# Kernel optimization log

Measured on AMD Instinct MI355X. Metric: run time of the kernel, lower is better.

## Reference

```python
import jax, jax.numpy as jnp
import numpy as np

N_NODES = 50000
N_EDGES = 800000
D_FEAT = 96


def setup_inputs() -> dict:
    key = jax.random.key(0)
    kx, ks, kd = jax.random.split(key, 3)
    x = jax.random.normal(kx, (N_NODES, D_FEAT), dtype=jnp.float32)
    src = jax.random.randint(ks, (N_EDGES,), 0, N_NODES, dtype=jnp.int64)
    dst = jax.random.randint(kd, (N_EDGES,), 0, N_NODES, dtype=jnp.int64)
    return {"x": x, "src": src, "dst": dst}


def reference(x, src, dst):
    n = x.shape[0]
    ones = jnp.ones(src.shape[0], dtype=x.dtype)
    # out-degree: edges leaving each node (src side)
    out_deg = jnp.clip(jax.ops.segment_sum(ones, src, num_segments=n), 1.0, None)
    # in-degree: edges arriving at each node (dst side)
    in_deg = jnp.clip(jax.ops.segment_sum(ones, dst, num_segments=n), 1.0, None)
    # pre-scale by out-degree^{-1/2}
    xs = x * (out_deg ** -0.5)[:, None]
    # copy_u + sum aggregation: sum messages from src into dst
    agg = jax.ops.segment_sum(xs[src], dst, num_segments=n)
    # post-scale by in-degree^{-1/2}
    return agg * (in_deg ** -0.5)[:, None]
```

## Files before the change

### kernel.cpp

```cpp
#include <hip/hip_runtime.h>


#define D_FEAT 96
#define CAP 64
#define PART_SHIFT 8
#define PNODES 256
#define NP_MAX 256
#define EPB 3328
#define EREG 13
#define OVF_CAP 8192

__device__ __forceinline__ unsigned short f2bf_rne(float f) {
    unsigned u = __float_as_uint(f);
    unsigned r = (u >> 16) & 1u;
    u += 0x7fffu + r;
    return (unsigned short)(u >> 16);
}


__global__ __launch_bounds__(256) void partition_kernel(
        const int* __restrict__ src, const int* __restrict__ dst,
        int n_edges, int np, int stride,
        int* __restrict__ pcur_d, int* __restrict__ pcur_s,
        unsigned* __restrict__ pbuf_d, unsigned short* __restrict__ pbuf_s,
        int* __restrict__ ctr,
        int* __restrict__ povf_d, int* __restrict__ sovf_d) {
    __shared__ int hcd[NP_MAX], hcs[NP_MAX];
    __shared__ int bd[NP_MAX], bs_[NP_MAX];
    __shared__ int od[NP_MAX], os_[NP_MAX];
    const int base = blockIdx.x * EPB;

    for (int i = threadIdx.x; i < NP_MAX; i += 256) {
        hcd[i] = 0; hcs[i] = 0; od[i] = 0; os_[i] = 0;
    }
    __syncthreads();

    unsigned v[EREG];
    #pragma unroll
    for (int k = 0; k < EREG; ++k) {
        int i = base + (int)threadIdx.x + (k << 8);
        if (i < n_edges) {
            int s = src[i], d = dst[i];
            unsigned pv = (unsigned)d | ((unsigned)s << 16);
            v[k] = pv;
            atomicAdd(&hcd[d >> PART_SHIFT], 1);
            atomicAdd(&hcs[s >> PART_SHIFT], 1);
        }
    }
    __syncthreads();

    for (int p = threadIdx.x; p < np; p += 256) {
        int cd = hcd[p];
        bd[p] = cd ? atomicAdd(&pcur_d[p], cd) : 0;
        int cs = hcs[p];
        bs_[p] = cs ? atomicAdd(&pcur_s[p], cs) : 0;
    }
    __syncthreads();

    #pragma unroll
    for (int k = 0; k < EREG; ++k) {
        int i = base + (int)threadIdx.x + (k << 8);
        if (i < n_edges) {
            unsigned pv = v[k];
            int d = (int)(pv & 0xffffu);
            int s = (int)(pv >> 16);
            int pd = d >> PART_SHIFT;
            int j = bd[pd] + atomicAdd(&od[pd], 1);
            if (j < stride) pbuf_d[(size_t)pd * stride + j] = pv;
            else { int k2 = atomicAdd(&ctr[1], 1); if (k2 < OVF_CAP) povf_d[k2] = (int)pv; }
            int ps = s >> PART_SHIFT;
            int j2 = bs_[ps] + atomicAdd(&os_[ps], 1);
            if (j2 < stride) pbuf_s[(size_t)ps * stride + j2] = (unsigned short)s;
            else { int k3 = atomicAdd(&ctr[2], 1); if (k3 < OVF_CAP) sovf_d[k3] = s; }
        }
    }
}


__global__ __launch_bounds__(256) void bincnt_kernel(
        const unsigned* __restrict__ pbuf_d, const int* __restrict__ pcur_d,
        const unsigned short* __restrict__ pbuf_s, const int* __restrict__ pcur_s,
        int stride, int n_nodes,
        const float* __restrict__ x, unsigned* __restrict__ xs,
        int* __restrict__ cursor, int* __restrict__ out_cnt,
        unsigned short* __restrict__ slots,
        int* __restrict__ ctr,
        const int* __restrict__ povf_d, const int* __restrict__ sovf_d,
        int* __restrict__ ovf_d) {
    __shared__ unsigned short lslots[PNODES * CAP];
    __shared__ int lcnt[PNODES];
    __shared__ int lout[PNODES];
    const int b = blockIdx.x;
    const int nbase = b << PART_SHIFT;
    const int nloc = min(PNODES, n_nodes - nbase);

    for (int i = threadIdx.x; i < PNODES; i += 256) { lcnt[i] = 0; lout[i] = 0; }
    __syncthreads();

    int n = pcur_d[b]; if (n > stride) n = stride;
    for (int i = threadIdx.x; i < n; i += 256) {
        unsigned pv = pbuf_d[(size_t)b * stride + i];
        int dl = (int)(pv & 0xffu);
        int s  = (int)(pv >> 16);
        int pos = atomicAdd(&lcnt[dl], 1);
        if (pos < CAP) lslots[dl * CAP + pos] = (unsigned short)s;
        else { int k = atomicAdd(&ctr[0], 1); if (k < OVF_CAP) ovf_d[k] = (int)pv; }
    }
    int n2 = pcur_s[b]; if (n2 > stride) n2 = stride;
    for (int i = threadIdx.x; i < n2; i += 256) {
        int s = (int)pbuf_s[(size_t)b * stride + i];
        atomicAdd(&lout[s & (PNODES - 1)], 1);
    }
    int npv = ctr[1];
    if (npv > 0) {
        if (npv > OVF_CAP) npv = OVF_CAP;
        for (int i = threadIdx.x; i < npv; i += 256) {
            unsigned pv = (unsigned)povf_d[i];
            int d = (int)(pv & 0xffffu);
            if ((d >> PART_SHIFT) == b) {
                int dl = d & (PNODES - 1);
                int pos = atomicAdd(&lcnt[dl], 1);
                if (pos < CAP) lslots[dl * CAP + pos] = (unsigned short)(pv >> 16);
                else { int k = atomicAdd(&ctr[0], 1); if (k < OVF_CAP) ovf_d[k] = (int)pv; }
            }
        }
    }
    int nsv = ctr[2];
    if (nsv > 0) {
        if (nsv > OVF_CAP) nsv = OVF_CAP;
        for (int i = threadIdx.x; i < nsv; i += 256) {
            int s = sovf_d[i];
            if ((s >> PART_SHIFT) == b) atomicAdd(&lout[s & (PNODES - 1)], 1);
        }
    }
    __syncthreads();

    for (int i = threadIdx.x; i < nloc; i += 256) {
        cursor[nbase + i]  = lcnt[i];
        out_cnt[nbase + i] = lout[i];
    }
    const unsigned* ls = (const unsigned*)lslots;
    unsigned* gs = (unsigned*)slots + (size_t)nbase * (CAP / 2);
    const int ncopy = nloc * (CAP / 2);
    for (int i = threadIdx.x; i < ncopy; i += 256) gs[i] = ls[i];

    const int ntot = nloc * 24;
    for (int i = threadIdx.x; i < ntot; i += 256) {
        int nd = i / 24;
        int j  = i - nd * 24;
        int c  = lout[nd];
        float w = rsqrtf((float)(c < 1 ? 1 : c));
        float4 vv = ((const float4*)(x + (size_t)(nbase + nd) * D_FEAT))[j];
        unsigned lo0 = f2bf_rne(vv.x * w), hi0 = f2bf_rne(vv.y * w);
        unsigned lo1 = f2bf_rne(vv.z * w), hi1 = f2bf_rne(vv.w * w);
        uint2 o;
        o.x = lo0 | (hi0 << 16);
        o.y = lo1 | (hi1 << 16);
        ((uint2*)(xs + (size_t)(nbase + nd) * 48))[j] = o;
    }
}


__global__ __launch_bounds__(256) void gather_kernel(
        const unsigned* __restrict__ xs,
        const unsigned short* __restrict__ slots,
        const int* __restrict__ cursor,
        const float* __restrict__ x,
        const int* __restrict__ out_cnt,
        const int* __restrict__ ctr,
        const int* __restrict__ ovf_d,
        float* __restrict__ out, int n_nodes) {
    int wid  = threadIdx.x >> 6;
    int lane = threadIdx.x & 63;
    int node = __builtin_amdgcn_readfirstlane(blockIdx.x * 4 + wid);
    if (node >= n_nodes) return;

    int cnt_all = __builtin_amdgcn_readfirstlane(cursor[node]);
    int cnt = cnt_all < CAP ? cnt_all : CAP;

    float accx = 0.f, accy = 0.f;
    const bool act = lane < 48;

    if (cnt > 0) {
        int idx  = lane < cnt ? lane : cnt - 1;
        int sval = (int)slots[node * CAP + idx];

        int e = 0;
        for (; e + 16 <= cnt; e += 16) {
            if (act) {
                unsigned u[16];
                #pragma unroll
                for (int k = 0; k < 16; ++k) {
                    int s = __builtin_amdgcn_readlane(sval, e + k);
                    u[k] = xs[s * 48 + lane];
                }
                #pragma unroll
                for (int k = 0; k < 16; ++k) {
                    accx += __uint_as_float(u[k] << 16);
                    accy += __uint_as_float(u[k] & 0xffff0000u);
                }
            }
        }
        for (; e + 4 <= cnt; e += 4) {
            if (act) {
                unsigned u[4];
                #pragma unroll
                for (int k = 0; k < 4; ++k) {
                    int s = __builtin_amdgcn_readlane(sval, e + k);
                    u[k] = xs[s * 48 + lane];
                }
                #pragma unroll
                for (int k = 0; k < 4; ++k) {
                    accx += __uint_as_float(u[k] << 16);
                    accy += __uint_as_float(u[k] & 0xffff0000u);
                }
            }
        }
        for (; e < cnt; ++e) {
            if (act) {
                int s = __builtin_amdgcn_readlane(sval, e);
                unsigned u0 = xs[s * 48 + lane];
                accx += __uint_as_float(u0 << 16);
                accy += __uint_as_float(u0 & 0xffff0000u);
            }
        }
    }

    if (cnt_all > CAP) {
        int novf = __builtin_amdgcn_readfirstlane(ctr[0]);
        if (novf > OVF_CAP) novf = OVF_CAP;
        for (int k = 0; k < novf; ++k) {
            unsigned pv = (unsigned)ovf_d[k];
            if ((int)(pv & 0xffffu) == node) {
                int s = (int)(pv >> 16);
                int c = out_cnt[s];
                float w = rsqrtf((float)(c < 1 ? 1 : c));
                if (act) {
                    accx += w * x[(size_t)s * D_FEAT + lane * 2];
                    accy += w * x[(size_t)s * D_FEAT + lane * 2 + 1];
                }
            }
        }
    }

    float sc = rsqrtf((float)(cnt_all < 1 ? 1 : cnt_all));
    if (act) {
        float* op = out + (size_t)node * D_FEAT + lane * 2;
        op[0] = accx * sc;
        op[1] = accy * sc;
    }
}


__global__ void degree_kernel(const int* __restrict__ src,
                              const int* __restrict__ dst,
                              int* __restrict__ out_cnt,
                              int* __restrict__ in_cnt, int n_edges) {
    int i = blockIdx.x * blockDim.x + threadIdx.x;
    if (i < n_edges) {
        atomicAdd(&out_cnt[src[i]], 1);
        atomicAdd(&in_cnt[dst[i]], 1);
    }
}

__global__ void scale_kernel(float* __restrict__ osc, float* __restrict__ isc, int n) {
    int i = blockIdx.x * blockDim.x + threadIdx.x;
    if (i < n) {
        int c0 = ((const int*)osc)[i];
        int c1 = ((const int*)isc)[i];
        osc[i] = rsqrtf((float)(c0 < 1 ? 1 : c0));
        isc[i] = rsqrtf((float)(c1 < 1 ? 1 : c1));
    }
}

__global__ void scatter_kernel(const float* __restrict__ x,
                               const int* __restrict__ src,
                               const int* __restrict__ dst,
                               const float* __restrict__ osc,
                               const float* __restrict__ isc,
                               float* __restrict__ out, int n_edges) {
    int idx = blockIdx.x * blockDim.x + threadIdx.x;
    int e = idx / 24, c = idx % 24;
    if (e >= n_edges) return;
    int s = src[e], d = dst[e];
    float w = osc[s] * isc[d];
    const float4 v = *(const float4*)(x + (size_t)s * D_FEAT + c * 4);
    float* o = out + (size_t)d * D_FEAT + c * 4;
    unsafeAtomicAdd(o + 0, v.x * w);
    unsafeAtomicAdd(o + 1, v.y * w);
    unsafeAtomicAdd(o + 2, v.z * w);
    unsafeAtomicAdd(o + 3, v.w * w);
}


extern "C" void kernel_launch(void* const* d_in, const int* in_sizes, int n_in,
                              void* d_out, int out_size, void* d_ws, size_t ws_size,
                              hipStream_t stream) {
    const float* x  = (const float*)d_in[0];
    const int* src  = (const int*)d_in[1];
    const int* dst  = (const int*)d_in[2];
    float* out      = (float*)d_out;

    const int n_edges = in_sizes[1];
    const int n_nodes = in_sizes[0] / D_FEAT;

    const int np = (n_nodes + PNODES - 1) / PNODES;
    const int avg = n_edges / (np > 0 ? np : 1);
    const int stride = avg + avg / 4 + 1024;
    const int pblocks = (n_edges + EPB - 1) / EPB;

    const size_t pbuf_words  = (size_t)np * stride;
    const size_t pbufs_words = (pbuf_words + 1) / 2;

    int* pcur_d  = (int*)d_ws;
    int* pcur_s  = pcur_d + 256;
    int* ctr     = pcur_d + 512;
    int* ovf_d   = pcur_d + 1024;
    int* povf_d  = ovf_d + OVF_CAP;
    int* sovf_d  = povf_d + OVF_CAP;
    int* out_cnt = sovf_d + OVF_CAP;
    int* cursor  = out_cnt + 65536;
    unsigned* pbuf_dst = (unsigned*)(cursor + 65536);
    unsigned short* pbuf_src = (unsigned short*)(pbuf_dst + pbuf_words);
    unsigned* xs = pbuf_dst + pbuf_words + pbufs_words;
    unsigned short* slots = (unsigned short*)(xs + (size_t)n_nodes * 48);

    const size_t needed = ((size_t)1024 + 3 * OVF_CAP + 2 * 65536 + pbuf_words +
                           pbufs_words + (size_t)n_nodes * 48 +
                           (size_t)n_nodes * (CAP / 2)) * 4;

    if (ws_size >= needed && n_nodes <= 65536 && np <= NP_MAX && pblocks <= 256) {
        (void)hipMemsetAsync(d_ws, 0, 1024 * sizeof(int), stream);

        partition_kernel<<<pblocks, 256, 0, stream>>>(
            src, dst, n_edges, np, stride, pcur_d, pcur_s,
            pbuf_dst, pbuf_src, ctr, povf_d, sovf_d);

        bincnt_kernel<<<np, 256, 0, stream>>>(
            pbuf_dst, pcur_d, pbuf_src, pcur_s, stride, n_nodes,
            x, xs, cursor, out_cnt, slots, ctr, povf_d, sovf_d, ovf_d);

        gather_kernel<<<(n_nodes + 3) / 4, 256, 0, stream>>>(
            xs, slots, cursor, x, out_cnt, ctr, ovf_d, out, n_nodes);
    } else {
        float* osc = (float*)d_ws;
        float* isc = osc + 65536;
        (void)hipMemsetAsync(d_ws, 0, 2 * 65536 * sizeof(int), stream);
        (void)hipMemsetAsync(d_out, 0, (size_t)out_size * sizeof(float), stream);
        degree_kernel<<<(n_edges + 255) / 256, 256, 0, stream>>>(
            src, dst, (int*)osc, (int*)isc, n_edges);
        scale_kernel<<<(n_nodes + 255) / 256, 256, 0, stream>>>(osc, isc, n_nodes);
        const int total = n_edges * 24;
        scatter_kernel<<<(total + 255) / 256, 256, 0, stream>>>(
            x, src, dst, osc, isc, out, n_edges);
    }
}
```

Before: 138.2 us.

## Replace global-cursor partition buffers with fixed per-block chunks

The partition kernel now writes each edge into a fixed-size chunk indexed by (partition, source block) with a per-block local counter. This removes the histogram pre-pass, the global atomic cursor reservation and a barrier. The bincnt kernel walks the chunks one wavefront per chunk using the stored counts. The trade-offs are sparse chunk occupancy, which means many partially used wavefronts and more scattered reads in bincnt, and an extra counts array.

```diff
diff --git a/kernel.cpp b/kernel.cpp
--- a/kernel.cpp
+++ b/kernel.cpp
@@ -7,7 +7,7 @@
 #define PNODES 256
 #define NP_MAX 256
 #define EPB 3328
-#define EREG 13
+#define CHK 48
 #define OVF_CAP 8192
 
 __device__ __forceinline__ unsigned short f2bf_rne(float f) {
@@ -20,67 +20,45 @@
 
 __global__ __launch_bounds__(256) void partition_kernel(
         const int* __restrict__ src, const int* __restrict__ dst,
-        int n_edges, int np, int stride,
-        int* __restrict__ pcur_d, int* __restrict__ pcur_s,
-        unsigned* __restrict__ pbuf_d, unsigned short* __restrict__ pbuf_s,
+        int n_edges, int np, int nblk,
+        int* __restrict__ counts_d, int* __restrict__ counts_s,
+        unsigned* __restrict__ pbuf_d,
+        unsigned short* __restrict__ pbuf_s,
         int* __restrict__ ctr,
         int* __restrict__ povf_d, int* __restrict__ sovf_d) {
-    __shared__ int hcd[NP_MAX], hcs[NP_MAX];
-    __shared__ int bd[NP_MAX], bs_[NP_MAX];
     __shared__ int od[NP_MAX], os_[NP_MAX];
-    const int base = blockIdx.x * EPB;
-
-    for (int i = threadIdx.x; i < NP_MAX; i += 256) {
-        hcd[i] = 0; hcs[i] = 0; od[i] = 0; os_[i] = 0;
-    }
+    const int blk = blockIdx.x;
+    const int base = blk * EPB;
+    const int end = min(base + EPB, n_edges);
+
+    for (int i = threadIdx.x; i < NP_MAX; i += 256) { od[i] = 0; os_[i] = 0; }
     __syncthreads();
 
-    unsigned v[EREG];
-    #pragma unroll
-    for (int k = 0; k < EREG; ++k) {
-        int i = base + (int)threadIdx.x + (k << 8);
-        if (i < n_edges) {
-            int s = src[i], d = dst[i];
-            unsigned pv = (unsigned)d | ((unsigned)s << 16);
-            v[k] = pv;
-            atomicAdd(&hcd[d >> PART_SHIFT], 1);
-            atomicAdd(&hcs[s >> PART_SHIFT], 1);
-        }
+    for (int i = base + (int)threadIdx.x; i < end; i += 256) {
+        int s = src[i], d = dst[i];
+        unsigned pv = (unsigned)d | ((unsigned)s << 16);
+        int pd = d >> PART_SHIFT;
+        int pos = atomicAdd(&od[pd], 1);
+        if (pos < CHK) pbuf_d[((size_t)pd * nblk + blk) * CHK + pos] = pv;
+        else { int k = atomicAdd(&ctr[1], 1); if (k < OVF_CAP) povf_d[k] = (int)pv; }
+        int ps = s >> PART_SHIFT;
+        int pos2 = atomicAdd(&os_[ps], 1);
+        if (pos2 < CHK) pbuf_s[((size_t)ps * nblk + blk) * CHK + pos2] = (unsigned short)s;
+        else { int k = atomicAdd(&ctr[2], 1); if (k < OVF_CAP) sovf_d[k] = s; }
     }
     __syncthreads();
 
     for (int p = threadIdx.x; p < np; p += 256) {
-        int cd = hcd[p];
-        bd[p] = cd ? atomicAdd(&pcur_d[p], cd) : 0;
-        int cs = hcs[p];
-        bs_[p] = cs ? atomicAdd(&pcur_s[p], cs) : 0;
-    }
-    __syncthreads();
-
-    #pragma unroll
-    for (int k = 0; k < EREG; ++k) {
-        int i = base + (int)threadIdx.x + (k << 8);
-        if (i < n_edges) {
-            unsigned pv = v[k];
-            int d = (int)(pv & 0xffffu);
-            int s = (int)(pv >> 16);
-            int pd = d >> PART_SHIFT;
-            int j = bd[pd] + atomicAdd(&od[pd], 1);
-            if (j < stride) pbuf_d[(size_t)pd * stride + j] = pv;
-            else { int k2 = atomicAdd(&ctr[1], 1); if (k2 < OVF_CAP) povf_d[k2] = (int)pv; }
-            int ps = s >> PART_SHIFT;
-            int j2 = bs_[ps] + atomicAdd(&os_[ps], 1);
-            if (j2 < stride) pbuf_s[(size_t)ps * stride + j2] = (unsigned short)s;
-            else { int k3 = atomicAdd(&ctr[2], 1); if (k3 < OVF_CAP) sovf_d[k3] = s; }
-        }
+        int cd = od[p];  counts_d[p * nblk + blk] = cd < CHK ? cd : CHK;
+        int cs = os_[p]; counts_s[p * nblk + blk] = cs < CHK ? cs : CHK;
     }
 }
 
 
 __global__ __launch_bounds__(256) void bincnt_kernel(
-        const unsigned* __restrict__ pbuf_d, const int* __restrict__ pcur_d,
-        const unsigned short* __restrict__ pbuf_s, const int* __restrict__ pcur_s,
-        int stride, int n_nodes,
+        const unsigned* __restrict__ pbuf_d, const int* __restrict__ counts_d,
+        const unsigned short* __restrict__ pbuf_s, const int* __restrict__ counts_s,
+        int nblk, int n_nodes,
         const float* __restrict__ x, unsigned* __restrict__ xs,
         int* __restrict__ cursor, int* __restrict__ out_cnt,
         unsigned short* __restrict__ slots,
@@ -93,23 +71,28 @@
     const int b = blockIdx.x;
     const int nbase = b << PART_SHIFT;
     const int nloc = min(PNODES, n_nodes - nbase);
+    const int wid  = threadIdx.x >> 6;
+    const int lane = threadIdx.x & 63;
 
     for (int i = threadIdx.x; i < PNODES; i += 256) { lcnt[i] = 0; lout[i] = 0; }
     __syncthreads();
 
-    int n = pcur_d[b]; if (n > stride) n = stride;
-    for (int i = threadIdx.x; i < n; i += 256) {
-        unsigned pv = pbuf_d[(size_t)b * stride + i];
-        int dl = (int)(pv & 0xffu);
-        int s  = (int)(pv >> 16);
-        int pos = atomicAdd(&lcnt[dl], 1);
-        if (pos < CAP) lslots[dl * CAP + pos] = (unsigned short)s;
-        else { int k = atomicAdd(&ctr[0], 1); if (k < OVF_CAP) ovf_d[k] = (int)pv; }
-    }
-    int n2 = pcur_s[b]; if (n2 > stride) n2 = stride;
-    for (int i = threadIdx.x; i < n2; i += 256) {
-        int s = (int)pbuf_s[(size_t)b * stride + i];
-        atomicAdd(&lout[s & (PNODES - 1)], 1);
+    for (int c = wid; c < nblk; c += 4) {
+        int cnt = __builtin_amdgcn_readfirstlane(counts_d[b * nblk + c]);
+        if (lane < cnt) {
+            unsigned pv = pbuf_d[((size_t)b * nblk + c) * CHK + lane];
+            int dl = (int)(pv & 0xffu);
+            int pos = atomicAdd(&lcnt[dl], 1);
+            if (pos < CAP) lslots[dl * CAP + pos] = (unsigned short)(pv >> 16);
+            else { int k = atomicAdd(&ctr[0], 1); if (k < OVF_CAP) ovf_d[k] = (int)pv; }
+        }
+    }
+    for (int c = wid; c < nblk; c += 4) {
+        int cnt = __builtin_amdgcn_readfirstlane(counts_s[b * nblk + c]);
+        if (lane < cnt) {
+            int s = (int)pbuf_s[((size_t)b * nblk + c) * CHK + lane];
+            atomicAdd(&lout[s & (PNODES - 1)], 1);
+        }
     }
     int npv = ctr[1];
     if (npv > 0) {
@@ -305,39 +288,38 @@
     const int n_nodes = in_sizes[0] / D_FEAT;
 
     const int np = (n_nodes + PNODES - 1) / PNODES;
-    const int avg = n_edges / (np > 0 ? np : 1);
-    const int stride = avg + avg / 4 + 1024;
-    const int pblocks = (n_edges + EPB - 1) / EPB;
-
-    const size_t pbuf_words  = (size_t)np * stride;
+    const int nblk = (n_edges + EPB - 1) / EPB;
+
+    const size_t chunks      = (size_t)np * nblk;
+    const size_t pbuf_words  = chunks * CHK;
     const size_t pbufs_words = (pbuf_words + 1) / 2;
 
-    int* pcur_d  = (int*)d_ws;
-    int* pcur_s  = pcur_d + 256;
-    int* ctr     = pcur_d + 512;
-    int* ovf_d   = pcur_d + 1024;
-    int* povf_d  = ovf_d + OVF_CAP;
-    int* sovf_d  = povf_d + OVF_CAP;
-    int* out_cnt = sovf_d + OVF_CAP;
-    int* cursor  = out_cnt + 65536;
-    unsigned* pbuf_dst = (unsigned*)(cursor + 65536);
+    int* ctr      = (int*)d_ws;
+    int* ovf_d    = ctr + 256;
+    int* povf_d   = ovf_d + OVF_CAP;
+    int* sovf_d   = povf_d + OVF_CAP;
+    int* out_cnt  = sovf_d + OVF_CAP;
+    int* cursor   = out_cnt + 65536;
+    int* counts_d = cursor + 65536;
+    int* counts_s = counts_d + chunks;
+    unsigned* pbuf_dst = (unsigned*)(counts_s + chunks);
     unsigned short* pbuf_src = (unsigned short*)(pbuf_dst + pbuf_words);
     unsigned* xs = pbuf_dst + pbuf_words + pbufs_words;
     unsigned short* slots = (unsigned short*)(xs + (size_t)n_nodes * 48);
 
-    const size_t needed = ((size_t)1024 + 3 * OVF_CAP + 2 * 65536 + pbuf_words +
-                           pbufs_words + (size_t)n_nodes * 48 +
+    const size_t needed = ((size_t)256 + 3 * OVF_CAP + 2 * 65536 + 2 * chunks +
+                           pbuf_words + pbufs_words + (size_t)n_nodes * 48 +
                            (size_t)n_nodes * (CAP / 2)) * 4;
 
-    if (ws_size >= needed && n_nodes <= 65536 && np <= NP_MAX && pblocks <= 256) {
-        (void)hipMemsetAsync(d_ws, 0, 1024 * sizeof(int), stream);
-
-        partition_kernel<<<pblocks, 256, 0, stream>>>(
-            src, dst, n_edges, np, stride, pcur_d, pcur_s,
+    if (ws_size >= needed && n_nodes <= 65536 && np <= NP_MAX && nblk <= 256) {
+        (void)hipMemsetAsync(d_ws, 0, 256 * sizeof(int), stream);
+
+        partition_kernel<<<nblk, 256, 0, stream>>>(
+            src, dst, n_edges, np, nblk, counts_d, counts_s,
             pbuf_dst, pbuf_src, ctr, povf_d, sovf_d);
 
         bincnt_kernel<<<np, 256, 0, stream>>>(
-            pbuf_dst, pcur_d, pbuf_src, pcur_s, stride, n_nodes,
+            pbuf_dst, counts_d, pbuf_src, counts_s, nblk, n_nodes,
             x, xs, cursor, out_cnt, slots, ctr, povf_d, sovf_d, ovf_d);
 
         gather_kernel<<<(n_nodes + 3) / 4, 256, 0, stream>>>(
```

Result: slower. 184.8 us (+33.8%).
